# Performance work log

Hardware: AMD Instinct MI355X
Metric: run time of the kernel (lower is better)

Reference implementation:

```python
import jax, jax.numpy as jnp
import numpy as np

D = 768
H = 16
DH = D // H  # 48
SCALE = 1.0 / np.sqrt(DH).astype(np.float32)
EPS = 1e-3  # keras LayerNormalization default epsilon
NEG = -1e9


def setup_inputs() -> dict:
    key = jax.random.key(0)
    ks = jax.random.split(key, 10)
    B, S = 4, 2048
    q = jax.random.normal(ks[0], (B, S, D), dtype=jnp.float32)
    k = jax.random.normal(ks[1], (B, S, D), dtype=jnp.float32)
    v = jax.random.normal(ks[2], (B, S, D), dtype=jnp.float32)
    # Dense projection params (glorot-ish scale)
    w_std = 1.0 / np.sqrt(D)
    Wq = jax.random.normal(ks[3], (D, D), dtype=jnp.float32) * w_std
    Wk = jax.random.normal(ks[4], (D, D), dtype=jnp.float32) * w_std
    Wv = jax.random.normal(ks[5], (D, D), dtype=jnp.float32) * w_std
    bq = jnp.zeros((D,), jnp.float32)
    bk = jnp.zeros((D,), jnp.float32)
    bv = jnp.zeros((D,), jnp.float32)
    gamma = jnp.ones((D,), jnp.float32)
    beta = jnp.zeros((D,), jnp.float32)
    return {"q": q, "k": k, "v": v, "Wq": Wq, "bq": bq, "Wk": Wk, "bk": bk,
            "Wv": Wv, "bv": bv, "gamma": gamma, "beta": beta}


def reference(q, k, v, Wq, bq, Wk, bk, Wv, bv, gamma, beta):
    use_causal = True  # exercise the causal-mask path
    B, S, _ = q.shape
    # Projections, then split into heads (tf.split on last axis == reshape)
    Q = (q @ Wq + bq).reshape(B, S, H, DH)
    K = (k @ Wk + bk).reshape(B, S, H, DH)
    V = (v @ Wv + bv).reshape(B, S, H, DH)
    # scores: [B, H, Sq, Sk]
    scores = jnp.einsum('bqhd,bkhd->bhqk', Q, K) * SCALE
    if use_causal:
        qi = jnp.arange(S)[:, None]
        ki = jnp.arange(S)[None, :]
        mask = jnp.where(qi >= ki, 0.0, NEG).astype(scores.dtype)
        scores = scores + mask
    attn = jax.nn.softmax(scores, axis=-1)
    out = jnp.einsum('bhqk,bkhd->bqhd', attn, V).reshape(B, S, D)
    # LayerNorm over last dim
    mu = jnp.mean(out, axis=-1, keepdims=True)
    var = jnp.mean(jnp.square(out - mu), axis=-1, keepdims=True)
    return (out - mu) * jax.lax.rsqrt(var + EPS) * gamma + beta
```

## Files before the change

### kernel.cpp

```cpp
#include <hip/hip_runtime.h>
#include <hip/hip_bf16.h>


#define DMODEL 768
#define NHEAD  16
#define DHEAD  48
#define SEQ    2048
#define NBATCH 4
#define NROWS  (NBATCH * SEQ)
#define QSCALE (0.14433756729740643f * 1.4426950408889634f)

typedef __bf16 bf16x8 __attribute__((ext_vector_type(8)));
typedef float  f32x4  __attribute__((ext_vector_type(4)));
typedef unsigned int u32x4 __attribute__((ext_vector_type(4)));

static __device__ __forceinline__ unsigned int pk2(float lo, float hi) {
    unsigned short a = __builtin_bit_cast(unsigned short, (__bf16)lo);
    unsigned short b = __builtin_bit_cast(unsigned short, (__bf16)hi);
    return ((unsigned int)b << 16) | a;
}

__global__ __launch_bounds__(256) void prep(
    const float* __restrict__ Wq,
    const float* __restrict__ Wk,
    const float* __restrict__ Wv,
    const float* __restrict__ xq,
    const float* __restrict__ xk,
    const float* __restrict__ xv,
    __hip_bfloat16* __restrict__ Wt,
    __hip_bfloat16* __restrict__ Xbq,
    __hip_bfloat16* __restrict__ Xbk,
    __hip_bfloat16* __restrict__ Xbv)
{
    int bid = blockIdx.x;
    if (bid < 1728) {
        __shared__ __hip_bfloat16 tile[32][33];
        int mat = bid / 576;
        int t   = bid - mat * 576;
        int tr  = t / 24, tc = t - (t / 24) * 24;
        const float* W = (mat == 0) ? Wq : (mat == 1) ? Wk : Wv;
        __hip_bfloat16* O = Wt + (size_t)mat * DMODEL * DMODEL;
        int tx = threadIdx.x & 31, ty = threadIdx.x >> 5;
#pragma unroll
        for (int i = 0; i < 32; i += 8)
            tile[ty + i][tx] = __float2bfloat16(W[(size_t)(tr * 32 + ty + i) * DMODEL + tc * 32 + tx]);
        __syncthreads();
#pragma unroll
        for (int i = 0; i < 32; i += 8)
            O[(size_t)(tc * 32 + ty + i) * DMODEL + tr * 32 + tx] = tile[tx][ty + i];
    } else {
        int b2  = bid - 1728;
        int mat = b2 / 3072;
        int r   = b2 - mat * 3072;
        const float* X = (mat == 0) ? xq : (mat == 1) ? xk : xv;
        __hip_bfloat16* O = (mat == 0) ? Xbq : (mat == 1) ? Xbk : Xbv;
        size_t off = (size_t)r * 2048 + threadIdx.x * 8;
        float4 f0 = *(const float4*)(X + off);
        float4 f1 = *(const float4*)(X + off + 4);
        unsigned int w0 = pk2(f0.x, f0.y), w1 = pk2(f0.z, f0.w);
        unsigned int w2 = pk2(f1.x, f1.y), w3 = pk2(f1.z, f1.w);
        u32x4 pv; pv[0] = w0; pv[1] = w1; pv[2] = w2; pv[3] = w3;
        *(u32x4*)(O + off) = pv;
    }
}

__global__ __launch_bounds__(512, 4) void qkv_proj(
    const __hip_bfloat16* __restrict__ Xbq,
    const __hip_bfloat16* __restrict__ Xbk,
    const __hip_bfloat16* __restrict__ Xbv,
    const __hip_bfloat16* __restrict__ Wt,
    const float* __restrict__ bq,
    const float* __restrict__ bk,
    const float* __restrict__ bv,
    __hip_bfloat16* __restrict__ Qr,
    __hip_bfloat16* __restrict__ Kr,
    __hip_bfloat16* __restrict__ Vt)
{
    __shared__ __hip_bfloat16 Abuf[3][8192];
    __shared__ __hip_bfloat16 Bbuf[2][4096];

    int tid  = threadIdx.x;
    int w    = tid >> 6, lane = tid & 63;
    int l16  = lane & 15, quad = lane >> 4;
    int wm   = w >> 1, wn = w & 1;

    int xcd = blockIdx.x & 7, s = blockIdx.x >> 3;
    int nt  = s % 6;
    int idx = (s / 6) * 8 + xcd;
    int mat = idx >> 5, mt = idx & 31;
    int m0  = mt * 256, n0 = nt * 128;

    const __hip_bfloat16* X = (mat == 0) ? Xbq : (mat == 1) ? Xbk : Xbv;
    const __hip_bfloat16* W = Wt + (size_t)mat * DMODEL * DMODEL;
    const float* bias       = (mat == 0) ? bq : (mat == 1) ? bk : bv;

    int sr = tid >> 2, sc = (tid & 3) * 8;
    const __hip_bfloat16* ga0 = X + (size_t)(m0 + sr) * DMODEL + sc;
    const __hip_bfloat16* ga1 = X + (size_t)(m0 + 128 + sr) * DMODEL + sc;
    const __hip_bfloat16* gb  = W + (size_t)(n0 + sr) * DMODEL + sc;

#define GLD(gp_, lp_) __builtin_amdgcn_global_load_lds(                        \
        (const __attribute__((address_space(1))) void*)(gp_),                  \
        (__attribute__((address_space(3))) void*)(lp_), 16, 0, 0)

    int aoff = (wm * 64 + l16) * 32 + quad * 8;
    int boff = (wn * 64 + l16) * 32 + quad * 8;

    f32x4 acc[4][4] = {};

    GLD(gb,       &Bbuf[0][tid * 8]);
    GLD(ga0,      &Abuf[0][tid * 8]);
    GLD(ga1,      &Abuf[0][4096 + tid * 8]);
    GLD(ga0 + 32, &Abuf[1][tid * 8]);
    GLD(ga1 + 32, &Abuf[1][4096 + tid * 8]);
    asm volatile("s_waitcnt vmcnt(2)" ::: "memory");
    asm volatile("s_barrier" ::: "memory");

    int abuf = 0, bbuf = 0, abS = 2;
    const __hip_bfloat16* gbS  = gb  + 32;
    const __hip_bfloat16* ga0S = ga0 + 64;
    const __hip_bfloat16* ga1S = ga1 + 64;

    for (int kt = 0; kt < 24; ++kt) {
        const __hip_bfloat16* LA = Abuf[abuf];
        const __hip_bfloat16* LB = Bbuf[bbuf];

        bf16x8 a[4], bA[2];
#pragma unroll
        for (int m_ = 0; m_ < 4; ++m_)
            a[m_] = *(const bf16x8*)&LA[aoff + m_ * 512];
        bA[0] = *(const bf16x8*)&LB[boff];
        bA[1] = *(const bf16x8*)&LB[boff + 512];

        if (kt < 23) { GLD(gbS, &Bbuf[bbuf ^ 1][tid * 8]); gbS += 32; }
        if (kt < 22) {
            GLD(ga0S, &Abuf[abS][tid * 8]);
            GLD(ga1S, &Abuf[abS][4096 + tid * 8]);
            ga0S += 32; ga1S += 32;
        }

        asm volatile("s_barrier" ::: "memory");
        __builtin_amdgcn_s_setprio(1);
#pragma unroll
        for (int m_ = 0; m_ < 4; ++m_) {
            acc[m_][0] = __builtin_amdgcn_mfma_f32_16x16x32_bf16(a[m_], bA[0], acc[m_][0], 0, 0, 0);
            acc[m_][1] = __builtin_amdgcn_mfma_f32_16x16x32_bf16(a[m_], bA[1], acc[m_][1], 0, 0, 0);
        }
        __builtin_amdgcn_s_setprio(0);
        asm volatile("s_barrier" ::: "memory");

        bf16x8 bB[2];
        bB[0] = *(const bf16x8*)&LB[boff + 1024];
        bB[1] = *(const bf16x8*)&LB[boff + 1536];

        if (kt < 22) asm volatile("s_waitcnt vmcnt(2)" ::: "memory");
        else         asm volatile("s_waitcnt vmcnt(0)" ::: "memory");
        asm volatile("s_barrier" ::: "memory");
        __builtin_amdgcn_s_setprio(1);
#pragma unroll
        for (int m_ = 0; m_ < 4; ++m_) {
            acc[m_][2] = __builtin_amdgcn_mfma_f32_16x16x32_bf16(a[m_], bB[0], acc[m_][2], 0, 0, 0);
            acc[m_][3] = __builtin_amdgcn_mfma_f32_16x16x32_bf16(a[m_], bB[1], acc[m_][3], 0, 0, 0);
        }
        __builtin_amdgcn_s_setprio(0);
        asm volatile("s_barrier" ::: "memory");

        abuf = (abuf == 2) ? 0 : abuf + 1;
        abS  = (abS  == 2) ? 0 : abS  + 1;
        bbuf ^= 1;
    }
#undef GLD

#pragma unroll
    for (int j = 0; j < 4; ++j) {
        int col = n0 + wn * 64 + j * 16 + l16;
        float bc = bias[col];
        if (mat == 0) {
#pragma unroll
            for (int i = 0; i < 4; ++i) {
                int row0 = m0 + wm * 64 + i * 16 + quad * 4;
#pragma unroll
                for (int r = 0; r < 4; ++r)
                    Qr[(size_t)(row0 + r) * DMODEL + col] =
                        __float2bfloat16((acc[i][j][r] + bc) * QSCALE);
            }
        } else if (mat == 1) {
#pragma unroll
            for (int i = 0; i < 4; ++i) {
                int row0 = m0 + wm * 64 + i * 16 + quad * 4;
#pragma unroll
                for (int r = 0; r < 4; ++r)
                    Kr[(size_t)(row0 + r) * DMODEL + col] =
                        __float2bfloat16(acc[i][j][r] + bc);
            }
        } else {
            int h = col / 48, dh = col - h * 48;
#pragma unroll
            for (int i = 0; i < 4; ++i) {
                int row0 = m0 + wm * 64 + i * 16 + quad * 4;
                int bb = row0 >> 11, s0 = row0 & 2047;
                unsigned int lo = pk2(acc[i][j][0] + bc, acc[i][j][1] + bc);
                unsigned int hi = pk2(acc[i][j][2] + bc, acc[i][j][3] + bc);
                uint2 pw; pw.x = lo; pw.y = hi;
                *(uint2*)(Vt + ((size_t)(bb * NHEAD + h) * DHEAD + dh) * SEQ + s0) = pw;
            }
        }
    }
}

__global__ __launch_bounds__(256, 3) void attn(
    const __hip_bfloat16* __restrict__ Qr,
    const __hip_bfloat16* __restrict__ Kr,
    const __hip_bfloat16* __restrict__ Vt,
    __hip_bfloat16* __restrict__ Ao)
{
    __shared__ __hip_bfloat16 Ks[2][64][64];
    __shared__ __hip_bfloat16 Vs[2][48][64];

    int tid  = threadIdx.x;
    int w    = tid >> 6, lane = tid & 63;
    int l16  = lane & 15, quad = lane >> 4;
    bool b1  = (quad & 2) != 0, b0 = (quad & 1) != 0;
    int bh   = blockIdx.x & 63;
    int qt   = 15 - (blockIdx.x >> 6);
    int q0   = qt * 128;
    int b    = bh >> 4, h = bh & 15;
    size_t rowbase = (size_t)b * SEQ;

    const __hip_bfloat16* Qp = Qr + rowbase * DMODEL + h * DHEAD;
    const __hip_bfloat16* Kp = Kr + rowbase * DMODEL + h * DHEAD;
    const __hip_bfloat16* Vp = Vt + (size_t)bh * DHEAD * SEQ;

    {
        int zbuf = tid >> 7, zr = (tid >> 1) & 63, zsl = 6 + (tid & 1);
        *(uint4*)&Ks[zbuf][zr][(zsl ^ (zr & 7)) * 8] = (uint4){0u, 0u, 0u, 0u};
    }

    int qb0 = q0 + w * 32, qb1 = qb0 + 16;
    bf16x8 bQa0, bQb0, bQa1, bQb1;
    {
        int qrow0 = qb0 + l16, qrow1 = qb1 + l16;
        bQa0 = *(const bf16x8*)(Qp + (size_t)qrow0 * DMODEL + quad * 8);
        bQa1 = *(const bf16x8*)(Qp + (size_t)qrow1 * DMODEL + quad * 8);
        bQb0 = (bf16x8){};
        bQb1 = (bf16x8){};
        if (quad < 2) {
            bQb0 = *(const bf16x8*)(Qp + (size_t)qrow0 * DMODEL + 32 + quad * 8);
            bQb1 = *(const bf16x8*)(Qp + (size_t)qrow1 * DMODEL + 32 + quad * 8);
        }
    }

    int kr1 = tid / 6,          ksl1 = tid - kr1 * 6;
    int kr2 = (tid + 256) / 6,  ksl2 = (tid + 256) - kr2 * 6;
    int vd1 = tid >> 3,         vsl1 = tid & 7;
    int vd2 = (tid + 256) >> 3, vsl2 = tid & 7;
    int kso1 = (ksl1 ^ (kr1 & 7)) * 8;
    int kso2 = (ksl2 ^ (kr2 & 7)) * 8;
    int vso1 = (vsl1 ^ (vd1 & 7)) * 8;
    int vso2 = (vsl2 ^ (vd2 & 7)) * 8;

    uint4 kv1, kv2, vv1, vv2;

#define ATTN_LOAD(kt_) {                                                        \
        int k0_ = (kt_) * 64;                                                   \
        kv1 = *(const uint4*)(Kp + (size_t)(k0_ + kr1) * DMODEL + ksl1 * 8);    \
        vv1 = *(const uint4*)(Vp + (size_t)vd1 * SEQ + k0_ + vsl1 * 8);         \
        if (tid < 128) {                                                        \
            kv2 = *(const uint4*)(Kp + (size_t)(k0_ + kr2) * DMODEL + ksl2 * 8);\
            vv2 = *(const uint4*)(Vp + (size_t)vd2 * SEQ + k0_ + vsl2 * 8);     \
        } }

#define ATTN_STORE(buf_) {                                                      \
        *(uint4*)&Ks[buf_][kr1][kso1] = kv1;                                    \
        *(uint4*)&Vs[buf_][vd1][vso1] = vv1;                                    \
        if (tid < 128) {                                                        \
            *(uint4*)&Ks[buf_][kr2][kso2] = kv2;                                \
            *(uint4*)&Vs[buf_][vd2][vso2] = vv2;                                \
        } }

#define EXPPK(sv_, uo0_, uo1_, ls_) {                                          \
        float p0 = exp2f(sv_[0]), p1 = exp2f(sv_[1]);                          \
        float p2 = exp2f(sv_[2]), p3 = exp2f(sv_[3]);                          \
        ls_ += (p0 + p1) + (p2 + p3);                                          \
        uo0_ = pk2(p0, p1); uo1_ = pk2(p2, p3); }

#define BFLY(u00,u01,u10,u11,u20,u21,u30,u31, P0v_, P1v_) {                    \
        unsigned int rA0 = __shfl_xor(b1 ? u00 : u10, 32, 64);                 \
        unsigned int rA1 = __shfl_xor(b1 ? u01 : u11, 32, 64);                 \
        unsigned int rB0 = __shfl_xor(b1 ? u20 : u30, 32, 64);                 \
        unsigned int rB1 = __shfl_xor(b1 ? u21 : u31, 32, 64);                 \
        unsigned int X00 = b1 ? rA0 : u00, X01 = b1 ? rA1 : u01;               \
        unsigned int X10 = b1 ? u10 : rA0, X11 = b1 ? u11 : rA1;               \
        unsigned int X20 = b1 ? rB0 : u20, X21 = b1 ? rB1 : u21;               \
        unsigned int X30 = b1 ? u30 : rB0, X31 = b1 ? u31 : rB1;               \
        unsigned int rC0 = __shfl_xor(b0 ? X00 : X10, 16, 64);                 \
        unsigned int rC1 = __shfl_xor(b0 ? X01 : X11, 16, 64);                 \
        unsigned int rD0 = __shfl_xor(b0 ? X20 : X30, 16, 64);                 \
        unsigned int rD1 = __shfl_xor(b0 ? X21 : X31, 16, 64);                 \
        u32x4 P0w, P1w;                                                        \
        P0w[0] = b0 ? rC0 : X00;  P0w[1] = b0 ? rC1 : X01;                     \
        P0w[2] = b0 ? X10 : rC0;  P0w[3] = b0 ? X11 : rC1;                     \
        P1w[0] = b0 ? rD0 : X20;  P1w[1] = b0 ? rD1 : X21;                     \
        P1w[2] = b0 ? X30 : rD0;  P1w[3] = b0 ? X31 : rD1;                     \
        P0v_ = __builtin_bit_cast(bf16x8, P0w);                                \
        P1v_ = __builtin_bit_cast(bf16x8, P1w); }

#define MFMA16(A_, B_, C_) __builtin_amdgcn_mfma_f32_16x16x32_bf16(A_, B_, C_, 0, 0, 0)

    f32x4 O00 = {}, O01 = {}, O02 = {}, O10 = {}, O11 = {}, O12 = {};
    float lsum0 = 0.f, lsum1 = 0.f;
    const f32x4 zf = {};

    int sA0 = (quad ^ (l16 & 7)) * 8;
    int sA1 = ((quad + 4) ^ (l16 & 7)) * 8;

    int ktmax = 2 * qt + 1;
    ATTN_LOAD(0);
    ATTN_STORE(0);
    if (ktmax >= 1) ATTN_LOAD(1);
    __syncthreads();

    for (int kt = 0; kt <= ktmax; ++kt) {
        int buf = kt & 1;
        int k0  = kt * 64;
        if (kt + 1 <= ktmax) ATTN_STORE(buf ^ 1);
        if (kt + 2 <= ktmax) ATTN_LOAD(kt + 2);

        bool do0 = (k0 <= qb0 + 15);
        bool do1 = (k0 <= qb1 + 15);

        f32x4 sA0_, sA1_, sA2_, sA3_, sB0_, sB1_, sB2_, sB3_;
        {
            bf16x8 aK00 = *(const bf16x8*)&Ks[buf][ 0 + l16][sA0];
            bf16x8 aK01 = *(const bf16x8*)&Ks[buf][16 + l16][sA0];
            bf16x8 aK02 = *(const bf16x8*)&Ks[buf][32 + l16][sA0];
            bf16x8 aK03 = *(const bf16x8*)&Ks[buf][48 + l16][sA0];
            bf16x8 aK10 = *(const bf16x8*)&Ks[buf][ 0 + l16][sA1];
            bf16x8 aK11 = *(const bf16x8*)&Ks[buf][16 + l16][sA1];
            bf16x8 aK12 = *(const bf16x8*)&Ks[buf][32 + l16][sA1];
            bf16x8 aK13 = *(const bf16x8*)&Ks[buf][48 + l16][sA1];
            __builtin_amdgcn_s_setprio(1);
            if (do0) {
                f32x4 z;
                z = MFMA16(aK00, bQa0, zf); sA0_ = MFMA16(aK10, bQb0, z);
                z = MFMA16(aK01, bQa0, zf); sA1_ = MFMA16(aK11, bQb0, z);
                z = MFMA16(aK02, bQa0, zf); sA2_ = MFMA16(aK12, bQb0, z);
                z = MFMA16(aK03, bQa0, zf); sA3_ = MFMA16(aK13, bQb0, z);
            }
            if (do1) {
                f32x4 z;
                z = MFMA16(aK00, bQa1, zf); sB0_ = MFMA16(aK10, bQb1, z);
                z = MFMA16(aK01, bQa1, zf); sB1_ = MFMA16(aK11, bQb1, z);
                z = MFMA16(aK02, bQa1, zf); sB2_ = MFMA16(aK12, bQb1, z);
                z = MFMA16(aK03, bQa1, zf); sB3_ = MFMA16(aK13, bQb1, z);
            }
            __builtin_amdgcn_s_setprio(0);
        }

        unsigned int a00, a01, a10, a11, a20, a21, a30, a31;
        unsigned int c00, c01, c10, c11, c20, c21, c30, c31;
        if (do0) {
            if (k0 + 63 > qb0) {
                int qg = qb0 + l16;
#pragma unroll
                for (int r = 0; r < 4; ++r) {
                    if (k0 +  0 + quad * 4 + r > qg) sA0_[r] = -1e30f;
                    if (k0 + 16 + quad * 4 + r > qg) sA1_[r] = -1e30f;
                    if (k0 + 32 + quad * 4 + r > qg) sA2_[r] = -1e30f;
                    if (k0 + 48 + quad * 4 + r > qg) sA3_[r] = -1e30f;
                }
            }
            float ls = 0.f;
            EXPPK(sA0_, a00, a01, ls);
            EXPPK(sA1_, a10, a11, ls);
            EXPPK(sA2_, a20, a21, ls);
            EXPPK(sA3_, a30, a31, ls);
            lsum0 += ls;
        }
        if (do1) {
            if (k0 + 63 > qb1) {
                int qg = qb1 + l16;
#pragma unroll
                for (int r = 0; r < 4; ++r) {
                    if (k0 +  0 + quad * 4 + r > qg) sB0_[r] = -1e30f;
                    if (k0 + 16 + quad * 4 + r > qg) sB1_[r] = -1e30f;
                    if (k0 + 32 + quad * 4 + r > qg) sB2_[r] = -1e30f;
                    if (k0 + 48 + quad * 4 + r > qg) sB3_[r] = -1e30f;
                }
            }
            float ls = 0.f;
            EXPPK(sB0_, c00, c01, ls);
            EXPPK(sB1_, c10, c11, ls);
            EXPPK(sB2_, c20, c21, ls);
            EXPPK(sB3_, c30, c31, ls);
            lsum1 += ls;
        }

        {
            bf16x8 bV00 = *(const bf16x8*)&Vs[buf][ 0 + l16][sA0];
            bf16x8 bV01 = *(const bf16x8*)&Vs[buf][16 + l16][sA0];
            bf16x8 bV02 = *(const bf16x8*)&Vs[buf][32 + l16][sA0];
            bf16x8 bV10 = *(const bf16x8*)&Vs[buf][ 0 + l16][sA1];
            bf16x8 bV11 = *(const bf16x8*)&Vs[buf][16 + l16][sA1];
            bf16x8 bV12 = *(const bf16x8*)&Vs[buf][32 + l16][sA1];

            if (do0) {
                bf16x8 P0v, P1v;
                BFLY(a00, a01, a10, a11, a20, a21, a30, a31, P0v, P1v);
                __builtin_amdgcn_s_setprio(1);
                O00 = MFMA16(P0v, bV00, O00); O00 = MFMA16(P1v, bV10, O00);
                O01 = MFMA16(P0v, bV01, O01); O01 = MFMA16(P1v, bV11, O01);
                O02 = MFMA16(P0v, bV02, O02); O02 = MFMA16(P1v, bV12, O02);
                __builtin_amdgcn_s_setprio(0);
            }
            if (do1) {
                bf16x8 P0v, P1v;
                BFLY(c00, c01, c10, c11, c20, c21, c30, c31, P0v, P1v);
                __builtin_amdgcn_s_setprio(1);
                O10 = MFMA16(P0v, bV00, O10); O10 = MFMA16(P1v, bV10, O10);
                O11 = MFMA16(P0v, bV01, O11); O11 = MFMA16(P1v, bV11, O11);
                O12 = MFMA16(P0v, bV02, O12); O12 = MFMA16(P1v, bV12, O12);
                __builtin_amdgcn_s_setprio(0);
            }
        }

        asm volatile("s_waitcnt lgkmcnt(0)" ::: "memory");
        __builtin_amdgcn_s_barrier();
        asm volatile("" ::: "memory");
    }

    lsum0 += __shfl_xor(lsum0, 16, 64);
    lsum0 += __shfl_xor(lsum0, 32, 64);
    lsum1 += __shfl_xor(lsum1, 16, 64);
    lsum1 += __shfl_xor(lsum1, 32, 64);

#pragma unroll
    for (int r = 0; r < 4; ++r) {
        {
            float linv = 1.f / __shfl(lsum0, quad * 4 + r, 64);
            size_t g = (rowbase + qb0 + quad * 4 + r) * DMODEL + h * DHEAD + l16;
            Ao[g + 0]  = __float2bfloat16(O00[r] * linv);
            Ao[g + 16] = __float2bfloat16(O01[r] * linv);
            Ao[g + 32] = __float2bfloat16(O02[r] * linv);
        }
        {
            float linv = 1.f / __shfl(lsum1, quad * 4 + r, 64);
            size_t g = (rowbase + qb1 + quad * 4 + r) * DMODEL + h * DHEAD + l16;
            Ao[g + 0]  = __float2bfloat16(O10[r] * linv);
            Ao[g + 16] = __float2bfloat16(O11[r] * linv);
            Ao[g + 32] = __float2bfloat16(O12[r] * linv);
        }
    }
#undef ATTN_LOAD
#undef ATTN_STORE
#undef EXPPK
#undef BFLY
#undef MFMA16
}

__global__ __launch_bounds__(256) void lnorm(
    const __hip_bfloat16* __restrict__ Ao,
    const float* __restrict__ gamma,
    const float* __restrict__ beta,
    float* __restrict__ out)
{
    int tid = threadIdx.x;
    int wv  = tid >> 6, ln = tid & 63;
    int row = blockIdx.x * 4 + wv;
    size_t base = (size_t)row * DMODEL + ln * 4;

    ushort4 u0 = *(const ushort4*)(Ao + base);
    ushort4 u1 = *(const ushort4*)(Ao + base + 256);
    ushort4 u2 = *(const ushort4*)(Ao + base + 512);
    float x0, x1, x2, x3, x4, x5, x6, x7, x8, x9, xa, xb;
    { unsigned int v = (unsigned int)u0.x << 16; __builtin_memcpy(&x0, &v, 4); }
    { unsigned int v = (unsigned int)u0.y << 16; __builtin_memcpy(&x1, &v, 4); }
    { unsigned int v = (unsigned int)u0.z << 16; __builtin_memcpy(&x2, &v, 4); }
    { unsigned int v = (unsigned int)u0.w << 16; __builtin_memcpy(&x3, &v, 4); }
    { unsigned int v = (unsigned int)u1.x << 16; __builtin_memcpy(&x4, &v, 4); }
    { unsigned int v = (unsigned int)u1.y << 16; __builtin_memcpy(&x5, &v, 4); }
    { unsigned int v = (unsigned int)u1.z << 16; __builtin_memcpy(&x6, &v, 4); }
    { unsigned int v = (unsigned int)u1.w << 16; __builtin_memcpy(&x7, &v, 4); }
    { unsigned int v = (unsigned int)u2.x << 16; __builtin_memcpy(&x8, &v, 4); }
    { unsigned int v = (unsigned int)u2.y << 16; __builtin_memcpy(&x9, &v, 4); }
    { unsigned int v = (unsigned int)u2.z << 16; __builtin_memcpy(&xa, &v, 4); }
    { unsigned int v = (unsigned int)u2.w << 16; __builtin_memcpy(&xb, &v, 4); }

    float s = ((x0 + x1) + (x2 + x3)) + ((x4 + x5) + (x6 + x7)) + ((x8 + x9) + (xa + xb));
    float q = ((x0*x0 + x1*x1) + (x2*x2 + x3*x3)) + ((x4*x4 + x5*x5) + (x6*x6 + x7*x7))
            + ((x8*x8 + x9*x9) + (xa*xa + xb*xb));
#pragma unroll
    for (int m = 32; m >= 1; m >>= 1) {
        s += __shfl_xor(s, m, 64);
        q += __shfl_xor(q, m, 64);
    }
    float mu  = s * (1.f / 768.f);
    float var = q * (1.f / 768.f) - mu * mu;
    float rstd = rsqrtf(var + 1e-3f);

    float4 g0 = *(const float4*)(gamma + ln * 4);
    float4 g1 = *(const float4*)(gamma + ln * 4 + 256);
    float4 g2 = *(const float4*)(gamma + ln * 4 + 512);
    float4 e0 = *(const float4*)(beta + ln * 4);
    float4 e1 = *(const float4*)(beta + ln * 4 + 256);
    float4 e2 = *(const float4*)(beta + ln * 4 + 512);
    float4 o0, o1, o2;
    o0.x = (x0 - mu) * rstd * g0.x + e0.x;
    o0.y = (x1 - mu) * rstd * g0.y + e0.y;
    o0.z = (x2 - mu) * rstd * g0.z + e0.z;
    o0.w = (x3 - mu) * rstd * g0.w + e0.w;
    o1.x = (x4 - mu) * rstd * g1.x + e1.x;
    o1.y = (x5 - mu) * rstd * g1.y + e1.y;
    o1.z = (x6 - mu) * rstd * g1.z + e1.z;
    o1.w = (x7 - mu) * rstd * g1.w + e1.w;
    o2.x = (x8 - mu) * rstd * g2.x + e2.x;
    o2.y = (x9 - mu) * rstd * g2.y + e2.y;
    o2.z = (xa - mu) * rstd * g2.z + e2.z;
    o2.w = (xb - mu) * rstd * g2.w + e2.w;
    *(float4*)(out + base)       = o0;
    *(float4*)(out + base + 256) = o1;
    *(float4*)(out + base + 512) = o2;
}

extern "C" void kernel_launch(void* const* d_in, const int* in_sizes, int n_in,
                              void* d_out, int out_size, void* d_ws, size_t ws_size,
                              hipStream_t stream) {
    const float* q     = (const float*)d_in[0];
    const float* k     = (const float*)d_in[1];
    const float* v     = (const float*)d_in[2];
    const float* Wq    = (const float*)d_in[3];
    const float* bq    = (const float*)d_in[4];
    const float* Wk    = (const float*)d_in[5];
    const float* bk    = (const float*)d_in[6];
    const float* Wv    = (const float*)d_in[7];
    const float* bv    = (const float*)d_in[8];
    const float* gamma = (const float*)d_in[9];
    const float* beta  = (const float*)d_in[10];

    char* basep = (char*)d_ws;
    __hip_bfloat16* Wt = (__hip_bfloat16*)basep;
    __hip_bfloat16* Qr = (__hip_bfloat16*)(basep + 3538944);
    __hip_bfloat16* Kr = Qr + (size_t)NROWS * DMODEL;
    __hip_bfloat16* Vt = Kr + (size_t)NROWS * DMODEL;
    __hip_bfloat16* Ao = Vt + (size_t)NROWS * DMODEL;
    float* out = (float*)d_out;

    __hip_bfloat16* Xbq = (__hip_bfloat16*)d_out;
    __hip_bfloat16* Xbk = Xbq + (size_t)NROWS * DMODEL;
    __hip_bfloat16* Xbv = Ao;

    hipLaunchKernelGGL(prep, dim3(10944), dim3(256), 0, stream,
                       Wq, Wk, Wv, q, k, v, Wt, Xbq, Xbk, Xbv);
    hipLaunchKernelGGL(qkv_proj, dim3(576), dim3(512), 0, stream,
                       Xbq, Xbk, Xbv, Wt, bq, bk, bv, Qr, Kr, Vt);
    hipLaunchKernelGGL(attn, dim3(1024), dim3(256), 0, stream, Qr, Kr, Vt, Ao);
    hipLaunchKernelGGL(lnorm, dim3(2048), dim3(256), 0, stream, Ao, gamma, beta, out);
}
```

Baseline: 270.4 us.

## Switch attention inner loop to 32x32x16 MFMA with ones-row softmax denominator

Rewrites the attention kernel's QK^T and PV products to use 32x32x16 bf16 MFMA tiles instead of 16x16x32. Each wave now handles 32 query rows per tile with a simpler single-stage shuffle. The softmax row sum is computed by padding V with a row of ones, so the MFMA accumulates the denominator and the scalar lsum adds and reductions go away. The cost is a larger V tile in LDS (64 rows instead of 48), wasted MFMA columns on padding, and a different causal-skip granularity.

```diff
diff --git a/kernel.cpp b/kernel.cpp
--- a/kernel.cpp
+++ b/kernel.cpp
@@ -12,6 +12,7 @@
 
 typedef __bf16 bf16x8 __attribute__((ext_vector_type(8)));
 typedef float  f32x4  __attribute__((ext_vector_type(4)));
+typedef float  f32x16 __attribute__((ext_vector_type(16)));
 typedef unsigned int u32x4 __attribute__((ext_vector_type(4)));
 
 static __device__ __forceinline__ unsigned int pk2(float lo, float hi) {
@@ -215,12 +216,13 @@
     __hip_bfloat16* __restrict__ Ao)
 {
     __shared__ __hip_bfloat16 Ks[2][64][64];
-    __shared__ __hip_bfloat16 Vs[2][48][64];
+    __shared__ __hip_bfloat16 Vs[2][64][64];
 
     int tid  = threadIdx.x;
     int w    = tid >> 6, lane = tid & 63;
-    int l16  = lane & 15, quad = lane >> 4;
-    bool b1  = (quad & 2) != 0, b0 = (quad & 1) != 0;
+    int l31  = lane & 31;
+    int half = lane >> 5;
+    bool hb  = half != 0;
     int bh   = blockIdx.x & 63;
     int qt   = 15 - (blockIdx.x >> 6);
     int q0   = qt * 128;
@@ -232,22 +234,20 @@
     const __hip_bfloat16* Vp = Vt + (size_t)bh * DHEAD * SEQ;
 
     {
-        int zbuf = tid >> 7, zr = (tid >> 1) & 63, zsl = 6 + (tid & 1);
-        *(uint4*)&Ks[zbuf][zr][(zsl ^ (zr & 7)) * 8] = (uint4){0u, 0u, 0u, 0u};
-    }
-
-    int qb0 = q0 + w * 32, qb1 = qb0 + 16;
-    bf16x8 bQa0, bQb0, bQa1, bQb1;
+        int zbuf = tid >> 7, zi = tid & 127;
+        int zr = 48 + (zi >> 3), zsl = zi & 7;
+        unsigned int v = (zr == 48) ? 0x3F803F80u : 0u;
+        u32x4 pv; pv[0] = v; pv[1] = v; pv[2] = v; pv[3] = v;
+        *(u32x4*)&Vs[zbuf][zr][(zsl ^ (zr & 7)) * 8] = pv;
+    }
+
+    int q0w = q0 + w * 32;
+    bf16x8 bQ0, bQ1, bQ2;
     {
-        int qrow0 = qb0 + l16, qrow1 = qb1 + l16;
-        bQa0 = *(const bf16x8*)(Qp + (size_t)qrow0 * DMODEL + quad * 8);
-        bQa1 = *(const bf16x8*)(Qp + (size_t)qrow1 * DMODEL + quad * 8);
-        bQb0 = (bf16x8){};
-        bQb1 = (bf16x8){};
-        if (quad < 2) {
-            bQb0 = *(const bf16x8*)(Qp + (size_t)qrow0 * DMODEL + 32 + quad * 8);
-            bQb1 = *(const bf16x8*)(Qp + (size_t)qrow1 * DMODEL + 32 + quad * 8);
-        }
+        const __hip_bfloat16* qp = Qp + (size_t)(q0w + l31) * DMODEL + half * 8;
+        bQ0 = *(const bf16x8*)(qp);
+        bQ1 = *(const bf16x8*)(qp + 16);
+        bQ2 = *(const bf16x8*)(qp + 32);
     }
 
     int kr1 = tid / 6,          ksl1 = tid - kr1 * 6;
@@ -278,41 +278,10 @@
             *(uint4*)&Vs[buf_][vd2][vso2] = vv2;                                \
         } }
 
-#define EXPPK(sv_, uo0_, uo1_, ls_) {                                          \
-        float p0 = exp2f(sv_[0]), p1 = exp2f(sv_[1]);                          \
-        float p2 = exp2f(sv_[2]), p3 = exp2f(sv_[3]);                          \
-        ls_ += (p0 + p1) + (p2 + p3);                                          \
-        uo0_ = pk2(p0, p1); uo1_ = pk2(p2, p3); }
-
-#define BFLY(u00,u01,u10,u11,u20,u21,u30,u31, P0v_, P1v_) {                    \
-        unsigned int rA0 = __shfl_xor(b1 ? u00 : u10, 32, 64);                 \
-        unsigned int rA1 = __shfl_xor(b1 ? u01 : u11, 32, 64);                 \
-        unsigned int rB0 = __shfl_xor(b1 ? u20 : u30, 32, 64);                 \
-        unsigned int rB1 = __shfl_xor(b1 ? u21 : u31, 32, 64);                 \
-        unsigned int X00 = b1 ? rA0 : u00, X01 = b1 ? rA1 : u01;               \
-        unsigned int X10 = b1 ? u10 : rA0, X11 = b1 ? u11 : rA1;               \
-        unsigned int X20 = b1 ? rB0 : u20, X21 = b1 ? rB1 : u21;               \
-        unsigned int X30 = b1 ? u30 : rB0, X31 = b1 ? u31 : rB1;               \
-        unsigned int rC0 = __shfl_xor(b0 ? X00 : X10, 16, 64);                 \
-        unsigned int rC1 = __shfl_xor(b0 ? X01 : X11, 16, 64);                 \
-        unsigned int rD0 = __shfl_xor(b0 ? X20 : X30, 16, 64);                 \
-        unsigned int rD1 = __shfl_xor(b0 ? X21 : X31, 16, 64);                 \
-        u32x4 P0w, P1w;                                                        \
-        P0w[0] = b0 ? rC0 : X00;  P0w[1] = b0 ? rC1 : X01;                     \
-        P0w[2] = b0 ? X10 : rC0;  P0w[3] = b0 ? X11 : rC1;                     \
-        P1w[0] = b0 ? rD0 : X20;  P1w[1] = b0 ? rD1 : X21;                     \
-        P1w[2] = b0 ? X30 : rD0;  P1w[3] = b0 ? X31 : rD1;                     \
-        P0v_ = __builtin_bit_cast(bf16x8, P0w);                                \
-        P1v_ = __builtin_bit_cast(bf16x8, P1w); }
-
-#define MFMA16(A_, B_, C_) __builtin_amdgcn_mfma_f32_16x16x32_bf16(A_, B_, C_, 0, 0, 0)
-
-    f32x4 O00 = {}, O01 = {}, O02 = {}, O10 = {}, O11 = {}, O12 = {};
-    float lsum0 = 0.f, lsum1 = 0.f;
-    const f32x4 zf = {};
-
-    int sA0 = (quad ^ (l16 & 7)) * 8;
-    int sA1 = ((quad + 4) ^ (l16 & 7)) * 8;
+#define MFMA32(A_, B_, C_) __builtin_amdgcn_mfma_f32_32x32x16_bf16(A_, B_, C_, 0, 0, 0)
+
+    f32x16 O1 = {}, O2 = {};
+    const f32x16 z16 = {};
 
     int ktmax = 2 * qt + 1;
     ATTN_LOAD(0);
@@ -326,100 +295,73 @@
         if (kt + 1 <= ktmax) ATTN_STORE(buf ^ 1);
         if (kt + 2 <= ktmax) ATTN_LOAD(kt + 2);
 
-        bool do0 = (k0 <= qb0 + 15);
-        bool do1 = (k0 <= qb1 + 15);
-
-        f32x4 sA0_, sA1_, sA2_, sA3_, sB0_, sB1_, sB2_, sB3_;
-        {
-            bf16x8 aK00 = *(const bf16x8*)&Ks[buf][ 0 + l16][sA0];
-            bf16x8 aK01 = *(const bf16x8*)&Ks[buf][16 + l16][sA0];
-            bf16x8 aK02 = *(const bf16x8*)&Ks[buf][32 + l16][sA0];
-            bf16x8 aK03 = *(const bf16x8*)&Ks[buf][48 + l16][sA0];
-            bf16x8 aK10 = *(const bf16x8*)&Ks[buf][ 0 + l16][sA1];
-            bf16x8 aK11 = *(const bf16x8*)&Ks[buf][16 + l16][sA1];
-            bf16x8 aK12 = *(const bf16x8*)&Ks[buf][32 + l16][sA1];
-            bf16x8 aK13 = *(const bf16x8*)&Ks[buf][48 + l16][sA1];
-            __builtin_amdgcn_s_setprio(1);
-            if (do0) {
-                f32x4 z;
-                z = MFMA16(aK00, bQa0, zf); sA0_ = MFMA16(aK10, bQb0, z);
-                z = MFMA16(aK01, bQa0, zf); sA1_ = MFMA16(aK11, bQb0, z);
-                z = MFMA16(aK02, bQa0, zf); sA2_ = MFMA16(aK12, bQb0, z);
-                z = MFMA16(aK03, bQa0, zf); sA3_ = MFMA16(aK13, bQb0, z);
-            }
-            if (do1) {
-                f32x4 z;
-                z = MFMA16(aK00, bQa1, zf); sB0_ = MFMA16(aK10, bQb1, z);
-                z = MFMA16(aK01, bQa1, zf); sB1_ = MFMA16(aK11, bQb1, z);
-                z = MFMA16(aK02, bQa1, zf); sB2_ = MFMA16(aK12, bQb1, z);
-                z = MFMA16(aK03, bQa1, zf); sB3_ = MFMA16(aK13, bQb1, z);
-            }
-            __builtin_amdgcn_s_setprio(0);
-        }
-
-        unsigned int a00, a01, a10, a11, a20, a21, a30, a31;
-        unsigned int c00, c01, c10, c11, c20, c21, c30, c31;
-        if (do0) {
-            if (k0 + 63 > qb0) {
-                int qg = qb0 + l16;
-#pragma unroll
-                for (int r = 0; r < 4; ++r) {
-                    if (k0 +  0 + quad * 4 + r > qg) sA0_[r] = -1e30f;
-                    if (k0 + 16 + quad * 4 + r > qg) sA1_[r] = -1e30f;
-                    if (k0 + 32 + quad * 4 + r > qg) sA2_[r] = -1e30f;
-                    if (k0 + 48 + quad * 4 + r > qg) sA3_[r] = -1e30f;
+#pragma unroll
+        for (int kc = 0; kc < 2; ++kc) {
+            int kbase = k0 + kc * 32;
+            if (kbase <= q0w + 31) {
+                int krow = kc * 32 + l31;
+                int ksw  = krow & 7;
+                bf16x8 aK0 = *(const bf16x8*)&Ks[buf][krow][((0 + half) ^ ksw) * 8];
+                bf16x8 aK1 = *(const bf16x8*)&Ks[buf][krow][((2 + half) ^ ksw) * 8];
+                bf16x8 aK2 = *(const bf16x8*)&Ks[buf][krow][((4 + half) ^ ksw) * 8];
+
+                __builtin_amdgcn_s_setprio(1);
+                f32x16 s_;
+                s_ = MFMA32(aK0, bQ0, z16);
+                s_ = MFMA32(aK1, bQ1, s_);
+                s_ = MFMA32(aK2, bQ2, s_);
+                __builtin_amdgcn_s_setprio(0);
+
+                if (kbase + 31 > q0w) {
+                    int qg = q0w + l31;
+                    int kb = kbase + (hb ? 4 : 0);
+#pragma unroll
+                    for (int r = 0; r < 16; ++r) {
+                        int kl = (r & 3) + 8 * (r >> 2);
+                        if (kb + kl > qg) s_[r] = -1e30f;
+                    }
                 }
-            }
-            float ls = 0.f;
-            EXPPK(sA0_, a00, a01, ls);
-            EXPPK(sA1_, a10, a11, ls);
-            EXPPK(sA2_, a20, a21, ls);
-            EXPPK(sA3_, a30, a31, ls);
-            lsum0 += ls;
-        }
-        if (do1) {
-            if (k0 + 63 > qb1) {
-                int qg = qb1 + l16;
-#pragma unroll
-                for (int r = 0; r < 4; ++r) {
-                    if (k0 +  0 + quad * 4 + r > qg) sB0_[r] = -1e30f;
-                    if (k0 + 16 + quad * 4 + r > qg) sB1_[r] = -1e30f;
-                    if (k0 + 32 + quad * 4 + r > qg) sB2_[r] = -1e30f;
-                    if (k0 + 48 + quad * 4 + r > qg) sB3_[r] = -1e30f;
+
+                unsigned int w0, w1, w2, w3, w4, w5, w6, w7;
+                {
+                    float e0 = exp2f(s_[0]),  e1 = exp2f(s_[1]);
+                    float e2 = exp2f(s_[2]),  e3 = exp2f(s_[3]);
+                    float e4 = exp2f(s_[4]),  e5 = exp2f(s_[5]);
+                    float e6 = exp2f(s_[6]),  e7 = exp2f(s_[7]);
+                    float e8 = exp2f(s_[8]),  e9 = exp2f(s_[9]);
+                    float ea = exp2f(s_[10]), eb = exp2f(s_[11]);
+                    float ec = exp2f(s_[12]), ed = exp2f(s_[13]);
+                    float ee = exp2f(s_[14]), ef = exp2f(s_[15]);
+                    w0 = pk2(e0, e1); w1 = pk2(e2, e3);
+                    w2 = pk2(e4, e5); w3 = pk2(e6, e7);
+                    w4 = pk2(e8, e9); w5 = pk2(ea, eb);
+                    w6 = pk2(ec, ed); w7 = pk2(ee, ef);
                 }
-            }
-            float ls = 0.f;
-            EXPPK(sB0_, c00, c01, ls);
-            EXPPK(sB1_, c10, c11, ls);
-            EXPPK(sB2_, c20, c21, ls);
-            EXPPK(sB3_, c30, c31, ls);
-            lsum1 += ls;
-        }
-
-        {
-            bf16x8 bV00 = *(const bf16x8*)&Vs[buf][ 0 + l16][sA0];
-            bf16x8 bV01 = *(const bf16x8*)&Vs[buf][16 + l16][sA0];
-            bf16x8 bV02 = *(const bf16x8*)&Vs[buf][32 + l16][sA0];
-            bf16x8 bV10 = *(const bf16x8*)&Vs[buf][ 0 + l16][sA1];
-            bf16x8 bV11 = *(const bf16x8*)&Vs[buf][16 + l16][sA1];
-            bf16x8 bV12 = *(const bf16x8*)&Vs[buf][32 + l16][sA1];
-
-            if (do0) {
-                bf16x8 P0v, P1v;
-                BFLY(a00, a01, a10, a11, a20, a21, a30, a31, P0v, P1v);
+
+                unsigned int sx0 = __shfl_xor(hb ? w0 : w2, 32, 64);
+                unsigned int sx1 = __shfl_xor(hb ? w1 : w3, 32, 64);
+                unsigned int sx2 = __shfl_xor(hb ? w4 : w6, 32, 64);
+                unsigned int sx3 = __shfl_xor(hb ? w5 : w7, 32, 64);
+                u32x4 F0w, F1w;
+                F0w[0] = hb ? sx0 : w0;  F0w[1] = hb ? sx1 : w1;
+                F0w[2] = hb ? w2  : sx0; F0w[3] = hb ? w3  : sx1;
+                F1w[0] = hb ? sx2 : w4;  F1w[1] = hb ? sx3 : w5;
+                F1w[2] = hb ? w6  : sx2; F1w[3] = hb ? w7  : sx3;
+                bf16x8 F0 = __builtin_bit_cast(bf16x8, F0w);
+                bf16x8 F1 = __builtin_bit_cast(bf16x8, F1w);
+
+                int vr0 = l31, vr1 = 32 + l31;
+                int vw0 = vr0 & 7, vw1 = vr1 & 7;
+                bf16x8 bV00 = *(const bf16x8*)&Vs[buf][vr0][((kc * 4 + 0 + half) ^ vw0) * 8];
+                bf16x8 bV01 = *(const bf16x8*)&Vs[buf][vr1][((kc * 4 + 0 + half) ^ vw1) * 8];
+                bf16x8 bV10 = *(const bf16x8*)&Vs[buf][vr0][((kc * 4 + 2 + half) ^ vw0) * 8];
+                bf16x8 bV11 = *(const bf16x8*)&Vs[buf][vr1][((kc * 4 + 2 + half) ^ vw1) * 8];
+
                 __builtin_amdgcn_s_setprio(1);
-                O00 = MFMA16(P0v, bV00, O00); O00 = MFMA16(P1v, bV10, O00);
-                O01 = MFMA16(P0v, bV01, O01); O01 = MFMA16(P1v, bV11, O01);
-                O02 = MFMA16(P0v, bV02, O02); O02 = MFMA16(P1v, bV12, O02);
-                __builtin_amdgcn_s_setprio(0);
-            }
-            if (do1) {
-                bf16x8 P0v, P1v;
-                BFLY(c00, c01, c10, c11, c20, c21, c30, c31, P0v, P1v);
-                __builtin_amdgcn_s_setprio(1);
-                O10 = MFMA16(P0v, bV00, O10); O10 = MFMA16(P1v, bV10, O10);
-                O11 = MFMA16(P0v, bV01, O11); O11 = MFMA16(P1v, bV11, O11);
-                O12 = MFMA16(P0v, bV02, O12); O12 = MFMA16(P1v, bV12, O12);
+                O1 = MFMA32(F0, bV00, O1);
+                O2 = MFMA32(F0, bV01, O2);
+                O1 = MFMA32(F1, bV10, O1);
+                O2 = MFMA32(F1, bV11, O2);
                 __builtin_amdgcn_s_setprio(0);
             }
         }
@@ -429,33 +371,20 @@
         asm volatile("" ::: "memory");
     }
 
-    lsum0 += __shfl_xor(lsum0, 16, 64);
-    lsum0 += __shfl_xor(lsum0, 32, 64);
-    lsum1 += __shfl_xor(lsum1, 16, 64);
-    lsum1 += __shfl_xor(lsum1, 32, 64);
-
-#pragma unroll
-    for (int r = 0; r < 4; ++r) {
-        {
-            float linv = 1.f / __shfl(lsum0, quad * 4 + r, 64);
-            size_t g = (rowbase + qb0 + quad * 4 + r) * DMODEL + h * DHEAD + l16;
-            Ao[g + 0]  = __float2bfloat16(O00[r] * linv);
-            Ao[g + 16] = __float2bfloat16(O01[r] * linv);
-            Ao[g + 32] = __float2bfloat16(O02[r] * linv);
-        }
-        {
-            float linv = 1.f / __shfl(lsum1, quad * 4 + r, 64);
-            size_t g = (rowbase + qb1 + quad * 4 + r) * DMODEL + h * DHEAD + l16;
-            Ao[g + 0]  = __float2bfloat16(O10[r] * linv);
-            Ao[g + 16] = __float2bfloat16(O11[r] * linv);
-            Ao[g + 32] = __float2bfloat16(O12[r] * linv);
-        }
+    int lsrc = (lane & 32) + 16;
+#pragma unroll
+    for (int r = 0; r < 16; ++r) {
+        float lden = __shfl(O2[r], lsrc, 64);
+        float linv = 1.f / lden;
+        int q = q0w + (r & 3) + 8 * (r >> 2) + (hb ? 4 : 0);
+        size_t g = (rowbase + q) * DMODEL + h * DHEAD;
+        Ao[g + l31] = __float2bfloat16(O1[r] * linv);
+        if (l31 < 16)
+            Ao[g + 32 + l31] = __float2bfloat16(O2[r] * linv);
     }
 #undef ATTN_LOAD
 #undef ATTN_STORE
-#undef EXPPK
-#undef BFLY
-#undef MFMA16
+#undef MFMA32
 }
 
 __global__ __launch_bounds__(256) void lnorm(
```

After: 260.6 us. -3.6%, faster.
